# Kernel optimization log

Measured on AMD Instinct MI355X. Metric: run time of the kernel, lower is better.

Reference implementation:

```python
import jax, jax.numpy as jnp
import numpy as np

N = 50000      # nodes
E = 800000     # edges (before self loops)
D_IN = 256
D_H = 256
D_OUT = 64     # num_classes
SLOPE = 0.01   # leaky_relu slope


def setup_inputs() -> dict:
    key = jax.random.key(0)
    ks = jax.random.split(key, 8)
    x = jax.random.normal(ks[0], (N, D_IN), dtype=jnp.float32)
    edge_index = jax.random.randint(ks[1], (2, E), 0, N, dtype=jnp.int32)
    s = 0.05
    W1 = jax.random.normal(ks[2], (D_H, D_IN), dtype=jnp.float32) * s
    b1 = jnp.zeros((D_H,), dtype=jnp.float32)
    W2 = jax.random.normal(ks[3], (D_H, D_H), dtype=jnp.float32) * s
    b2 = jnp.zeros((D_H,), dtype=jnp.float32)
    W3 = jax.random.normal(ks[4], (D_OUT, D_H), dtype=jnp.float32) * s
    b3 = jnp.zeros((D_OUT,), dtype=jnp.float32)
    return {"x": x, "edge_index": edge_index, "W1": W1, "b1": b1,
            "W2": W2, "b2": b2, "W3": W3, "b3": b3}


def _gcn_layer(x, W, b, src, dst):
    # PyG GCNConv: h = x @ W^T; out[dst] += d^{-1/2}[src] d^{-1/2}[dst] * h[src]; out += b
    h = x @ W.T                                             # [N, out]
    ones = jnp.ones(src.shape[0], dtype=h.dtype)
    deg = jax.ops.segment_sum(ones, dst, num_segments=N)    # includes self loops
    dinv = jnp.where(deg > 0, jax.lax.rsqrt(deg), 0.0)
    norm = dinv[src] * dinv[dst]                            # [E+N]
    msg = h[src] * norm[:, None]                            # gather + scale
    out = jax.ops.segment_sum(msg, dst, num_segments=N)     # scatter-add
    return out + b


def reference(x, edge_index, W1, b1, W2, b2, W3, b3):
    src, dst = edge_index[0], edge_index[1]
    loop = jnp.arange(N, dtype=src.dtype)                   # add self loops
    src = jnp.concatenate([src, loop])
    dst = jnp.concatenate([dst, loop])
    act = lambda h: jax.nn.leaky_relu(h, negative_slope=SLOPE)
    h1 = act(_gcn_layer(x, W1, b1, src, dst))
    h2 = act(_gcn_layer(h1, W2, b2, src, dst))
    logits = _gcn_layer(h2, W3, b3, src, dst)               # no activation on last layer
    return (h1, h2, logits)
```

## Files before the change

kernel.cpp:

```cpp
#include <hip/hip_runtime.h>

#define N_NODES 50000
#define E_EDGES 800000
#define SLOPE 0.01f
#define CSTRIDE 32

typedef __attribute__((ext_vector_type(8))) short bf16x8;
typedef __attribute__((ext_vector_type(4))) float floatx4;
typedef __attribute__((ext_vector_type(4))) float f32x4;
typedef __attribute__((ext_vector_type(2))) float f32x2;
typedef __attribute__((ext_vector_type(2))) unsigned int u32x2;

__device__ __forceinline__ unsigned short f2bf(float f) {
    unsigned u = __builtin_bit_cast(unsigned, f);
    unsigned r = (u + 0x7FFFu + ((u >> 16) & 1u)) >> 16;
    return (unsigned short)r;
}
__device__ __forceinline__ float bf2f(unsigned short h) {
    unsigned u = ((unsigned)h) << 16;
    return __builtin_bit_cast(float, u);
}
__device__ __forceinline__ float blo(unsigned u) { return __builtin_bit_cast(float, u << 16); }
__device__ __forceinline__ float bhi(unsigned u) { return __builtin_bit_cast(float, u & 0xFFFF0000u); }
__device__ __forceinline__ f32x2 up2(unsigned u) {
    f32x2 t; t.x = blo(u); t.y = bhi(u); return t;
}

__device__ __forceinline__ void acc8p(uint4 v, f32x2 a[4]) {
    a[0] += up2(v.x); a[1] += up2(v.y); a[2] += up2(v.z); a[3] += up2(v.w);
}
__device__ __forceinline__ void acc4p(uint2 v, f32x2 a[2]) {
    a[0] += up2(v.x); a[1] += up2(v.y);
}


__device__ __forceinline__ void conv_body(const float* __restrict__ in,
                                          unsigned short* __restrict__ out, int i, int n4) {
    if (i < n4) {
        float4 v = ((const float4*)in)[i];
        ushort4 o;
        o.x = f2bf(v.x); o.y = f2bf(v.y); o.z = f2bf(v.z); o.w = f2bf(v.w);
        ((ushort4*)out)[i] = o;
    }
}

__device__ __forceinline__ void wfrag_body(const float* __restrict__ Wf,
                                           unsigned short* __restrict__ out, int idx, int n4) {
    if (idx >= n4) return;
    int n = idx >> 6;
    int k = (idx & 63) << 2;
    float4 v = ((const float4*)Wf)[idx];
    int jt = n >> 4, lm = n & 15, kk = k >> 5, q = (k >> 3) & 3, e = k & 7;
    int off = ((jt * 8 + kk) * 64 + q * 16 + lm) * 8 + e;
    ushort4 o;
    o.x = f2bf(v.x); o.y = f2bf(v.y); o.z = f2bf(v.z); o.w = f2bf(v.w);
    *(ushort4*)(out + off) = o;
}

#define PREP_HIST_B   3125
#define PREP_CONV_B   12500
#define PREP_W1_B     64
#define PREP_W2_B     64
#define PREP_W3_B     16
#define PREP_TOTAL_B  (PREP_HIST_B + PREP_CONV_B + PREP_W1_B + PREP_W2_B + PREP_W3_B)

__global__ __launch_bounds__(256) void prep0_kernel(
        const float* __restrict__ x, unsigned short* __restrict__ xb,
        const float* __restrict__ W1, unsigned short* __restrict__ W1f,
        const float* __restrict__ W2, unsigned short* __restrict__ W2f,
        const float* __restrict__ W3, unsigned short* __restrict__ W3f,
        const int* __restrict__ dst, int* __restrict__ counts,
        unsigned short* __restrict__ rank) {
    int b = blockIdx.x, tid = threadIdx.x;
    if (b < PREP_HIST_B) {
        int e = b * 256 + tid;
        if (e < E_EDGES) {
            int d = dst[e];
            rank[e] = (unsigned short)atomicAdd(&counts[(size_t)d * CSTRIDE], 1);
        }
    } else if (b < PREP_HIST_B + PREP_CONV_B) {
        conv_body(x, xb, (b - PREP_HIST_B) * 256 + tid, N_NODES * 256 / 4);
    } else if (b < PREP_HIST_B + PREP_CONV_B + PREP_W1_B) {
        wfrag_body(W1, W1f, (b - PREP_HIST_B - PREP_CONV_B) * 256 + tid, 16384);
    } else if (b < PREP_HIST_B + PREP_CONV_B + PREP_W1_B + PREP_W2_B) {
        wfrag_body(W2, W2f, (b - PREP_HIST_B - PREP_CONV_B - PREP_W1_B) * 256 + tid, 16384);
    } else {
        wfrag_body(W3, W3f, (b - PREP_HIST_B - PREP_CONV_B - PREP_W1_B - PREP_W2_B) * 256 + tid, 4096);
    }
}


#define SB 1024
__global__ __launch_bounds__(SB) void scan1_dinv_kernel(const int* __restrict__ counts,
                                                        int* __restrict__ partial,
                                                        int* __restrict__ bsum,
                                                        float* __restrict__ dinv) {
    __shared__ int wsum[16];
    int tid = threadIdx.x, lane = tid & 63, wid = tid >> 6;
    int i = blockIdx.x * SB + tid;
    int v = (i < N_NODES) ? counts[(size_t)i * CSTRIDE] : 0;
    int x = v;
    #pragma unroll
    for (int off = 1; off < 64; off <<= 1) {
        int y = __shfl_up(x, off, 64);
        if (lane >= off) x += y;
    }
    if (lane == 63) wsum[wid] = x;
    __syncthreads();
    if (wid == 0) {
        int s = (lane < 16) ? wsum[lane] : 0;
        #pragma unroll
        for (int off = 1; off < 16; off <<= 1) {
            int y = __shfl_up(s, off, 64);
            if (lane >= off) s += y;
        }
        if (lane < 16) wsum[lane] = s;
    }
    __syncthreads();
    int woff = wid ? wsum[wid - 1] : 0;
    if (i < N_NODES) {
        partial[i] = woff + x - v;
        dinv[i] = rsqrtf((float)(v + 1));
    }
    if (tid == SB - 1) bsum[blockIdx.x] = woff + x;
}

__global__ __launch_bounds__(256) void scan3b_kernel(int* __restrict__ row_ptr,
                                                     const int* __restrict__ bsum,
                                                     int nb) {
    __shared__ int pref[64];
    int tid = threadIdx.x;
    if (tid < 64) {
        int v = (tid < nb) ? bsum[tid] : 0;
        #pragma unroll
        for (int off = 1; off < 64; off <<= 1) {
            int y = __shfl_up(v, off, 64);
            if (tid >= off) v += y;
        }
        pref[tid] = v;
    }
    __syncthreads();
    int i = blockIdx.x * 256 + tid;
    if (i < N_NODES) {
        int c = i >> 10;
        int off = c ? pref[c - 1] : 0;
        row_ptr[i] += off;
    }
    if (i == 0) row_ptr[N_NODES] = pref[nb - 1];
}


template<int WAVES_M, int WAVES_N, int MT, int NT>
__device__ __forceinline__ void gemm_frag_body(
        int bx, int by, int tid,
        const unsigned short* __restrict__ Ab,
        const unsigned short* __restrict__ Bf,
        const float* __restrict__ dinv,
        unsigned short* __restrict__ C, int M, int Nc) {
    const int wave = tid >> 6, lane = tid & 63;
    const int lm = lane & 15, q = lane >> 4;
    const int bm = bx * (WAVES_M * MT * 16);
    const int bn = by * (WAVES_N * NT * 16);
    const int wm = (wave / WAVES_N) * (MT * 16);
    const int wn = (wave % WAVES_N) * (NT * 16);
    const int jt0 = (bn + wn) >> 4;

    const unsigned short* arow[MT];
    #pragma unroll
    for (int i = 0; i < MT; ++i) {
        int r = bm + wm + i * 16 + lm;
        if (r >= M) r = M - 1;
        arow[i] = Ab + (size_t)r * 256 + q * 8;
    }

    floatx4 acc[MT][NT] = {};

    #pragma unroll
    for (int kk = 0; kk < 8; ++kk) {
        bf16x8 a[MT], b[NT];
        #pragma unroll
        for (int i = 0; i < MT; ++i)
            a[i] = *(const bf16x8*)(arow[i] + kk * 32);
        #pragma unroll
        for (int j = 0; j < NT; ++j)
            b[j] = *(const bf16x8*)(Bf + (((jt0 + j) * 8 + kk) * 64 + lane) * 8);
        #pragma unroll
        for (int i = 0; i < MT; ++i)
            #pragma unroll
            for (int j = 0; j < NT; ++j)
                acc[i][j] = __builtin_amdgcn_mfma_f32_16x16x32_bf16(a[i], b[j], acc[i][j], 0, 0, 0);
    }

    #pragma unroll
    for (int i = 0; i < MT; ++i) {
        int rb = bm + wm + i * 16 + q * 4;
        #pragma unroll
        for (int r = 0; r < 4; ++r) {
            int row = rb + r;
            if (row < M) {
                float dd = dinv[row];
                #pragma unroll
                for (int j = 0; j < NT; ++j)
                    C[(size_t)row * Nc + bn + wn + j * 16 + lm] = f2bf(acc[i][j][r] * dd);
            }
        }
    }
}

__global__ __launch_bounds__(256) void gemm256_kernel(
        const unsigned short* __restrict__ Ab, const unsigned short* __restrict__ Bf,
        const float* __restrict__ dinv, unsigned short* __restrict__ C, int M, int Nc) {
    gemm_frag_body<2, 2, 4, 4>(blockIdx.x, blockIdx.y, threadIdx.x, Ab, Bf, dinv, C, M, Nc);
}

__global__ __launch_bounds__(256) void gemm64_kernel(
        const unsigned short* __restrict__ Ab, const unsigned short* __restrict__ Bf,
        const float* __restrict__ dinv, unsigned short* __restrict__ C, int M, int Nc) {
    gemm_frag_body<4, 1, 4, 4>(blockIdx.x, 0, threadIdx.x, Ab, Bf, dinv, C, M, Nc);
}

#define GEMM1_B 782
__global__ __launch_bounds__(256) void gemm1_place_kernel(
        const unsigned short* __restrict__ Ab, const unsigned short* __restrict__ Bf,
        const float* __restrict__ dinv, unsigned short* __restrict__ C, int M, int Nc,
        const int* __restrict__ src, const int* __restrict__ dst,
        const int* __restrict__ row_ptr, const unsigned short* __restrict__ rank,
        int* __restrict__ col_idx) {
    int b = blockIdx.x;
    if (b < PREP_HIST_B) {
        int e = b * 256 + threadIdx.x;
        if (e < E_EDGES) {
            int d = dst[e];
            int pos = row_ptr[d] + (int)rank[e];
            col_idx[pos] = src[e];
        }
    } else {
        int b2 = b - PREP_HIST_B;
        gemm_frag_body<2, 2, 4, 4>(b2 >> 1, b2 & 1, threadIdx.x, Ab, Bf, dinv, C, M, Nc);
    }
}


template<bool ACT>
__global__ __launch_bounds__(256) void agg256_kernel(
        const int* __restrict__ row_ptr, const int* __restrict__ col_idx,
        const float* __restrict__ dinv, const unsigned short* __restrict__ hs,
        const float* __restrict__ bias,
        float* __restrict__ out, unsigned short* __restrict__ outb) {
    int node = __builtin_amdgcn_readfirstlane(blockIdx.x * 4 + (threadIdx.x >> 6));
    int lane = threadIdx.x & 63;
    int half = lane >> 5, sl = lane & 31;

    f32x2 a[4] = {};

    int beg = row_ptr[node], end = row_ptr[node + 1];
    int j = beg;
    for (; j + 8 <= end; j += 8) {
        int s0 = col_idx[j + half];
        int s1 = col_idx[j + 2 + half];
        int s2 = col_idx[j + 4 + half];
        int s3 = col_idx[j + 6 + half];
        uint4 v0 = ((const uint4*)(hs + (size_t)s0 * 256))[sl];
        uint4 v1 = ((const uint4*)(hs + (size_t)s1 * 256))[sl];
        uint4 v2 = ((const uint4*)(hs + (size_t)s2 * 256))[sl];
        uint4 v3 = ((const uint4*)(hs + (size_t)s3 * 256))[sl];
        acc8p(v0, a); acc8p(v1, a); acc8p(v2, a); acc8p(v3, a);
    }
    for (; j + 2 <= end; j += 2) {
        int s = col_idx[j + half];
        uint4 v = ((const uint4*)(hs + (size_t)s * 256))[sl];
        acc8p(v, a);
    }
    if (j < end && half == 0) {
        int s = col_idx[j];
        uint4 v = ((const uint4*)(hs + (size_t)s * 256))[sl];
        acc8p(v, a);
    }

    float s0 = a[0].x, s1 = a[0].y, s2 = a[1].x, s3 = a[1].y;
    float s4 = a[2].x, s5 = a[2].y, s6 = a[3].x, s7 = a[3].y;

    s0 += __shfl_xor(s0, 32); s1 += __shfl_xor(s1, 32);
    s2 += __shfl_xor(s2, 32); s3 += __shfl_xor(s3, 32);
    s4 += __shfl_xor(s4, 32); s5 += __shfl_xor(s5, 32);
    s6 += __shfl_xor(s6, 32); s7 += __shfl_xor(s7, 32);

    uint4 sv = ((const uint4*)(hs + (size_t)node * 256))[sl];
    s0 += blo(sv.x); s1 += bhi(sv.x);
    s2 += blo(sv.y); s3 += bhi(sv.y);
    s4 += blo(sv.z); s5 += bhi(sv.z);
    s6 += blo(sv.w); s7 += bhi(sv.w);

    int srcl = lane >> 1;
    float t0 = __shfl(s0, srcl), t1 = __shfl(s1, srcl);
    float t2 = __shfl(s2, srcl), t3 = __shfl(s3, srcl);
    float t4 = __shfl(s4, srcl), t5 = __shfl(s5, srcl);
    float t6 = __shfl(s6, srcl), t7 = __shfl(s7, srcl);
    bool hi = (lane & 1);
    float f0 = hi ? t4 : t0, f1 = hi ? t5 : t1, f2 = hi ? t6 : t2, f3 = hi ? t7 : t3;

    float dd = dinv[node];
    const float4 b4 = ((const float4*)bias)[lane];
    f0 = fmaf(f0, dd, b4.x); f1 = fmaf(f1, dd, b4.y);
    f2 = fmaf(f2, dd, b4.z); f3 = fmaf(f3, dd, b4.w);
    if (ACT) {
        f0 = f0 > 0.f ? f0 : SLOPE * f0;
        f1 = f1 > 0.f ? f1 : SLOPE * f1;
        f2 = f2 > 0.f ? f2 : SLOPE * f2;
        f3 = f3 > 0.f ? f3 : SLOPE * f3;
    }
    f32x4 o = {f0, f1, f2, f3};
    __builtin_nontemporal_store(o, (f32x4*)(out + (size_t)node * 256) + lane);
    u32x2 obv;
    obv.x = ((unsigned)f2bf(f1) << 16) | f2bf(f0);
    obv.y = ((unsigned)f2bf(f3) << 16) | f2bf(f2);
    ((u32x2*)(outb + (size_t)node * 256))[lane] = obv;
}

__global__ __launch_bounds__(256) void agg64_kernel(
        const int* __restrict__ row_ptr, const int* __restrict__ col_idx,
        const float* __restrict__ dinv, const unsigned short* __restrict__ hs,
        const float* __restrict__ bias, float* __restrict__ out) {
    int node = __builtin_amdgcn_readfirstlane(blockIdx.x * 4 + (threadIdx.x >> 6));
    int lane = threadIdx.x & 63;
    int g = lane >> 4, sl = lane & 15;

    f32x2 a[2] = {};

    int beg = row_ptr[node], end = row_ptr[node + 1];
    int j = beg;
    for (; j + 8 <= end; j += 8) {
        int s0 = col_idx[j + g];
        int s1 = col_idx[j + 4 + g];
        uint2 v0 = ((const uint2*)(hs + (size_t)s0 * 64))[sl];
        uint2 v1 = ((const uint2*)(hs + (size_t)s1 * 64))[sl];
        acc4p(v0, a); acc4p(v1, a);
    }
    for (; j + 4 <= end; j += 4) {
        int s = col_idx[j + g];
        uint2 v = ((const uint2*)(hs + (size_t)s * 64))[sl];
        acc4p(v, a);
    }
    int rem = end - j;
    if (g < rem) {
        int s = col_idx[j + g];
        uint2 v = ((const uint2*)(hs + (size_t)s * 64))[sl];
        acc4p(v, a);
    }

    float s0 = a[0].x, s1 = a[0].y, s2 = a[1].x, s3 = a[1].y;

    s0 += __shfl_xor(s0, 16); s0 += __shfl_xor(s0, 32);
    s1 += __shfl_xor(s1, 16); s1 += __shfl_xor(s1, 32);
    s2 += __shfl_xor(s2, 16); s2 += __shfl_xor(s2, 32);
    s3 += __shfl_xor(s3, 16); s3 += __shfl_xor(s3, 32);

    uint2 sv = ((const uint2*)(hs + (size_t)node * 64))[sl];
    s0 += blo(sv.x); s1 += bhi(sv.x);
    s2 += blo(sv.y); s3 += bhi(sv.y);

    float dd = dinv[node];
    const float4 b4 = ((const float4*)bias)[sl];
    f32x4 o;
    o[0] = fmaf(s0, dd, b4.x);
    o[1] = fmaf(s1, dd, b4.y);
    o[2] = fmaf(s2, dd, b4.z);
    o[3] = fmaf(s3, dd, b4.w);
    if (g == 0)
        __builtin_nontemporal_store(o, (f32x4*)(out + (size_t)node * 64) + sl);
}


static inline int cdiv(long long a, long long b) { return (int)((a + b - 1) / b); }

extern "C" void kernel_launch(void* const* d_in, const int* in_sizes, int n_in,
                              void* d_out, int out_size, void* d_ws, size_t ws_size,
                              hipStream_t stream) {
    const float* x  = (const float*)d_in[0];
    const int* ei   = (const int*)d_in[1];
    const float* W1 = (const float*)d_in[2];
    const float* b1 = (const float*)d_in[3];
    const float* W2 = (const float*)d_in[4];
    const float* b2 = (const float*)d_in[5];
    const float* W3 = (const float*)d_in[6];
    const float* b3 = (const float*)d_in[7];

    const int* src = ei;
    const int* dst = ei + E_EDGES;

    char* ws = (char*)d_ws;
    int*   row_ptr = (int*)ws;   ws += 50112 * 4;
    float* dinv    = (float*)ws; ws += 50048 * 4;
    int*   bsum    = (int*)ws;   ws += 64 * 4;
    unsigned short* rank = (unsigned short*)ws; ws += (size_t)E_EDGES * 2;
    int*   col_idx = (int*)ws;   ws += (size_t)E_EDGES * 4;
    unsigned short* W1f = (unsigned short*)ws; ws += 65536 * 2;
    unsigned short* W2f = (unsigned short*)ws; ws += 65536 * 2;
    unsigned short* W3f = (unsigned short*)ws; ws += 16384 * 2;
    unsigned short* hb  = (unsigned short*)ws; ws += (size_t)N_NODES * 256 * 2;
    unsigned short* ob  = (unsigned short*)ws;

    int* counts = (int*)hb;

    float* out1 = (float*)d_out;
    float* out2 = out1 + (size_t)N_NODES * 256;
    float* out3 = out2 + (size_t)N_NODES * 256;

    const int NB = cdiv(N_NODES, SB);

    (void)hipMemsetAsync(counts, 0, (size_t)50048 * CSTRIDE * sizeof(int), stream);
    prep0_kernel<<<PREP_TOTAL_B, 256, 0, stream>>>(x, ob, W1, W1f, W2, W2f, W3, W3f,
                                                   dst, counts, rank);

    scan1_dinv_kernel<<<NB, SB, 0, stream>>>(counts, row_ptr, bsum, dinv);
    scan3b_kernel<<<cdiv(N_NODES, 256), 256, 0, stream>>>(row_ptr, bsum, NB);

    dim3 g256(cdiv(N_NODES, 128), 2);
    int agg_grid = cdiv(N_NODES, 4);

    gemm1_place_kernel<<<PREP_HIST_B + GEMM1_B, 256, 0, stream>>>(
        ob, W1f, dinv, hb, N_NODES, 256, src, dst, row_ptr, rank, col_idx);
    agg256_kernel<true><<<agg_grid, 256, 0, stream>>>(row_ptr, col_idx, dinv, hb, b1, out1, ob);

    gemm256_kernel<<<g256, 256, 0, stream>>>(ob, W2f, dinv, hb, N_NODES, 256);
    agg256_kernel<true><<<agg_grid, 256, 0, stream>>>(row_ptr, col_idx, dinv, hb, b2, out2, ob);

    gemm64_kernel<<<cdiv(N_NODES, 256), 256, 0, stream>>>(ob, W3f, dinv, hb, N_NODES, 64);
    agg64_kernel<<<agg_grid, 256, 0, stream>>>(row_ptr, col_idx, dinv, hb, b3, out3);
}
```

Measured before the change: 425.4 us.

## Fuse fp32-to-bf16 conversion into layer-1 GEMM and overlap it with degree histogram

The first GEMM now reads fp32 x directly and converts it to bf16 in registers, which removes the separate conversion pass and the bf16 copy of x. Because the GEMM no longer needs dinv, it runs in the same launch as the degree histogram, and the per-source degree scaling for layer 1 moves into the aggregation as a per-edge dinv gather. Edge placement becomes its own kernel, and the padded per-node atomic counters are packed densely. The trade-offs are extra dinv loads per edge in the first aggregation, more atomic contention on adjacent counters, and GEMM blocks reading fp32 rows directly from global memory.

Measured after the change: 426.2 us. About the same (+0.2%).

```diff
diff --git a/kernel.cpp b/kernel.cpp
--- a/kernel.cpp
+++ b/kernel.cpp
@@ -3,7 +3,6 @@
 #define N_NODES 50000
 #define E_EDGES 800000
 #define SLOPE 0.01f
-#define CSTRIDE 32
 
 typedef __attribute__((ext_vector_type(8))) short bf16x8;
 typedef __attribute__((ext_vector_type(4))) float floatx4;
@@ -32,16 +31,10 @@
 __device__ __forceinline__ void acc4p(uint2 v, f32x2 a[2]) {
     a[0] += up2(v.x); a[1] += up2(v.y);
 }
-
-
-__device__ __forceinline__ void conv_body(const float* __restrict__ in,
-                                          unsigned short* __restrict__ out, int i, int n4) {
-    if (i < n4) {
-        float4 v = ((const float4*)in)[i];
-        ushort4 o;
-        o.x = f2bf(v.x); o.y = f2bf(v.y); o.z = f2bf(v.z); o.w = f2bf(v.w);
-        ((ushort4*)out)[i] = o;
-    }
+__device__ __forceinline__ void acc8f(uint4 v, float d, f32x2 a[4]) {
+    f32x2 dv; dv.x = d; dv.y = d;
+    a[0] += up2(v.x) * dv; a[1] += up2(v.y) * dv;
+    a[2] += up2(v.z) * dv; a[3] += up2(v.w) * dv;
 }
 
 __device__ __forceinline__ void wfrag_body(const float* __restrict__ Wf,
@@ -57,35 +50,96 @@
     *(ushort4*)(out + off) = o;
 }
 
-#define PREP_HIST_B   3125
-#define PREP_CONV_B   12500
-#define PREP_W1_B     64
-#define PREP_W2_B     64
-#define PREP_W3_B     16
-#define PREP_TOTAL_B  (PREP_HIST_B + PREP_CONV_B + PREP_W1_B + PREP_W2_B + PREP_W3_B)
-
-__global__ __launch_bounds__(256) void prep0_kernel(
-        const float* __restrict__ x, unsigned short* __restrict__ xb,
+__global__ __launch_bounds__(256) void prep_w_kernel(
         const float* __restrict__ W1, unsigned short* __restrict__ W1f,
         const float* __restrict__ W2, unsigned short* __restrict__ W2f,
-        const float* __restrict__ W3, unsigned short* __restrict__ W3f,
+        const float* __restrict__ W3, unsigned short* __restrict__ W3f) {
+    int b = blockIdx.x, tid = threadIdx.x;
+    if (b < 64)       wfrag_body(W1, W1f, b * 256 + tid, 16384);
+    else if (b < 128) wfrag_body(W2, W2f, (b - 64) * 256 + tid, 16384);
+    else              wfrag_body(W3, W3f, (b - 128) * 256 + tid, 4096);
+}
+
+
+__device__ __forceinline__ void gemm1x_body(
+        int bx, int by, int tid,
+        const float* __restrict__ X,
+        const unsigned short* __restrict__ Bf,
+        unsigned short* __restrict__ C, int M, int Nc) {
+    const int wave = tid >> 6, lane = tid & 63;
+    const int lm = lane & 15, q = lane >> 4;
+    const int bm = bx * 128;
+    const int bn = by * 128;
+    const int wm = (wave >> 1) * 64;
+    const int wn = (wave & 1) * 64;
+    const int jt0 = (bn + wn) >> 4;
+
+    const float* xr[4];
+    #pragma unroll
+    for (int i = 0; i < 4; ++i) {
+        int r = bm + wm + i * 16 + lm;
+        if (r >= M) r = M - 1;
+        xr[i] = X + (size_t)r * 256 + q * 8;
+    }
+
+    floatx4 acc[4][4] = {};
+
+    #pragma unroll
+    for (int kk = 0; kk < 8; ++kk) {
+        bf16x8 a[4], b[4];
+        #pragma unroll
+        for (int i = 0; i < 4; ++i) {
+            float4 v0 = *(const float4*)(xr[i] + kk * 32);
+            float4 v1 = *(const float4*)(xr[i] + kk * 32 + 4);
+            bf16x8 t;
+            t[0] = (short)f2bf(v0.x); t[1] = (short)f2bf(v0.y);
+            t[2] = (short)f2bf(v0.z); t[3] = (short)f2bf(v0.w);
+            t[4] = (short)f2bf(v1.x); t[5] = (short)f2bf(v1.y);
+            t[6] = (short)f2bf(v1.z); t[7] = (short)f2bf(v1.w);
+            a[i] = t;
+        }
+        #pragma unroll
+        for (int j = 0; j < 4; ++j)
+            b[j] = *(const bf16x8*)(Bf + (((jt0 + j) * 8 + kk) * 64 + lane) * 8);
+        #pragma unroll
+        for (int i = 0; i < 4; ++i)
+            #pragma unroll
+            for (int j = 0; j < 4; ++j)
+                acc[i][j] = __builtin_amdgcn_mfma_f32_16x16x32_bf16(a[i], b[j], acc[i][j], 0, 0, 0);
+    }
+
+    #pragma unroll
+    for (int i = 0; i < 4; ++i) {
+        int rb = bm + wm + i * 16 + q * 4;
+        #pragma unroll
+        for (int r = 0; r < 4; ++r) {
+            int row = rb + r;
+            if (row < M) {
+                #pragma unroll
+                for (int j = 0; j < 4; ++j)
+                    C[(size_t)row * Nc + bn + wn + j * 16 + lm] = f2bf(acc[i][j][r]);
+            }
+        }
+    }
+}
+
+#define HIST_B 3125
+#define G1X_B  782
+__global__ __launch_bounds__(256) void gemm1x_hist_kernel(
+        const float* __restrict__ x, const unsigned short* __restrict__ W1f,
+        unsigned short* __restrict__ hb,
         const int* __restrict__ dst, int* __restrict__ counts,
         unsigned short* __restrict__ rank) {
-    int b = blockIdx.x, tid = threadIdx.x;
-    if (b < PREP_HIST_B) {
-        int e = b * 256 + tid;
+    int b = blockIdx.x;
+    if (b < HIST_B) {
+        int e = b * 256 + threadIdx.x;
         if (e < E_EDGES) {
             int d = dst[e];
-            rank[e] = (unsigned short)atomicAdd(&counts[(size_t)d * CSTRIDE], 1);
-        }
-    } else if (b < PREP_HIST_B + PREP_CONV_B) {
-        conv_body(x, xb, (b - PREP_HIST_B) * 256 + tid, N_NODES * 256 / 4);
-    } else if (b < PREP_HIST_B + PREP_CONV_B + PREP_W1_B) {
-        wfrag_body(W1, W1f, (b - PREP_HIST_B - PREP_CONV_B) * 256 + tid, 16384);
-    } else if (b < PREP_HIST_B + PREP_CONV_B + PREP_W1_B + PREP_W2_B) {
-        wfrag_body(W2, W2f, (b - PREP_HIST_B - PREP_CONV_B - PREP_W1_B) * 256 + tid, 16384);
+            rank[e] = (unsigned short)atomicAdd(&counts[d], 1);
+        }
     } else {
-        wfrag_body(W3, W3f, (b - PREP_HIST_B - PREP_CONV_B - PREP_W1_B - PREP_W2_B) * 256 + tid, 4096);
+        int b2 = b - HIST_B;
+        gemm1x_body(b2 >> 1, b2 & 1, threadIdx.x, x, W1f, hb, N_NODES, 256);
     }
 }
 
@@ -98,7 +152,7 @@
     __shared__ int wsum[16];
     int tid = threadIdx.x, lane = tid & 63, wid = tid >> 6;
     int i = blockIdx.x * SB + tid;
-    int v = (i < N_NODES) ? counts[(size_t)i * CSTRIDE] : 0;
+    int v = (i < N_NODES) ? counts[i] : 0;
     int x = v;
     #pragma unroll
     for (int off = 1; off < 64; off <<= 1) {
@@ -147,6 +201,17 @@
         row_ptr[i] += off;
     }
     if (i == 0) row_ptr[N_NODES] = pref[nb - 1];
+}
+
+__global__ __launch_bounds__(256) void place_kernel(
+        const int* __restrict__ src, const int* __restrict__ dst,
+        const int* __restrict__ row_ptr, const unsigned short* __restrict__ rank,
+        int* __restrict__ col_idx) {
+    int e = blockIdx.x * 256 + threadIdx.x;
+    if (e < E_EDGES) {
+        int d = dst[e];
+        col_idx[row_ptr[d] + (int)rank[e]] = src[e];
+    }
 }
 
 
@@ -219,29 +284,8 @@
     gemm_frag_body<4, 1, 4, 4>(blockIdx.x, 0, threadIdx.x, Ab, Bf, dinv, C, M, Nc);
 }
 
-#define GEMM1_B 782
-__global__ __launch_bounds__(256) void gemm1_place_kernel(
-        const unsigned short* __restrict__ Ab, const unsigned short* __restrict__ Bf,
-        const float* __restrict__ dinv, unsigned short* __restrict__ C, int M, int Nc,
-        const int* __restrict__ src, const int* __restrict__ dst,
-        const int* __restrict__ row_ptr, const unsigned short* __restrict__ rank,
-        int* __restrict__ col_idx) {
-    int b = blockIdx.x;
-    if (b < PREP_HIST_B) {
-        int e = b * 256 + threadIdx.x;
-        if (e < E_EDGES) {
-            int d = dst[e];
-            int pos = row_ptr[d] + (int)rank[e];
-            col_idx[pos] = src[e];
-        }
-    } else {
-        int b2 = b - PREP_HIST_B;
-        gemm_frag_body<2, 2, 4, 4>(b2 >> 1, b2 & 1, threadIdx.x, Ab, Bf, dinv, C, M, Nc);
-    }
-}
-
-
-template<bool ACT>
+
+template<bool ACT, bool ESCALE>
 __global__ __launch_bounds__(256) void agg256_kernel(
         const int* __restrict__ row_ptr, const int* __restrict__ col_idx,
         const float* __restrict__ dinv, const unsigned short* __restrict__ hs,
@@ -251,6 +295,7 @@
     int lane = threadIdx.x & 63;
     int half = lane >> 5, sl = lane & 31;
 
+    float dd = dinv[node];
     f32x2 a[4] = {};
 
     int beg = row_ptr[node], end = row_ptr[node + 1];
@@ -264,17 +309,22 @@
         uint4 v1 = ((const uint4*)(hs + (size_t)s1 * 256))[sl];
         uint4 v2 = ((const uint4*)(hs + (size_t)s2 * 256))[sl];
         uint4 v3 = ((const uint4*)(hs + (size_t)s3 * 256))[sl];
-        acc8p(v0, a); acc8p(v1, a); acc8p(v2, a); acc8p(v3, a);
+        if (ESCALE) {
+            acc8f(v0, dinv[s0], a); acc8f(v1, dinv[s1], a);
+            acc8f(v2, dinv[s2], a); acc8f(v3, dinv[s3], a);
+        } else {
+            acc8p(v0, a); acc8p(v1, a); acc8p(v2, a); acc8p(v3, a);
+        }
     }
     for (; j + 2 <= end; j += 2) {
         int s = col_idx[j + half];
         uint4 v = ((const uint4*)(hs + (size_t)s * 256))[sl];
-        acc8p(v, a);
+        if (ESCALE) acc8f(v, dinv[s], a); else acc8p(v, a);
     }
     if (j < end && half == 0) {
         int s = col_idx[j];
         uint4 v = ((const uint4*)(hs + (size_t)s * 256))[sl];
-        acc8p(v, a);
+        if (ESCALE) acc8f(v, dinv[s], a); else acc8p(v, a);
     }
 
     float s0 = a[0].x, s1 = a[0].y, s2 = a[1].x, s3 = a[1].y;
@@ -286,10 +336,11 @@
     s6 += __shfl_xor(s6, 32); s7 += __shfl_xor(s7, 32);
 
     uint4 sv = ((const uint4*)(hs + (size_t)node * 256))[sl];
-    s0 += blo(sv.x); s1 += bhi(sv.x);
-    s2 += blo(sv.y); s3 += bhi(sv.y);
-    s4 += blo(sv.z); s5 += bhi(sv.z);
-    s6 += blo(sv.w); s7 += bhi(sv.w);
+    float sf = ESCALE ? dd : 1.0f;
+    s0 = fmaf(blo(sv.x), sf, s0); s1 = fmaf(bhi(sv.x), sf, s1);
+    s2 = fmaf(blo(sv.y), sf, s2); s3 = fmaf(bhi(sv.y), sf, s3);
+    s4 = fmaf(blo(sv.z), sf, s4); s5 = fmaf(bhi(sv.z), sf, s5);
+    s6 = fmaf(blo(sv.w), sf, s6); s7 = fmaf(bhi(sv.w), sf, s7);
 
     int srcl = lane >> 1;
     float t0 = __shfl(s0, srcl), t1 = __shfl(s1, srcl);
@@ -299,7 +350,6 @@
     bool hi = (lane & 1);
     float f0 = hi ? t4 : t0, f1 = hi ? t5 : t1, f2 = hi ? t6 : t2, f3 = hi ? t7 : t3;
 
-    float dd = dinv[node];
     const float4 b4 = ((const float4*)bias)[lane];
     f0 = fmaf(f0, dd, b4.x); f1 = fmaf(f1, dd, b4.y);
     f2 = fmaf(f2, dd, b4.z); f3 = fmaf(f3, dd, b4.w);
@@ -400,7 +450,7 @@
     unsigned short* hb  = (unsigned short*)ws; ws += (size_t)N_NODES * 256 * 2;
     unsigned short* ob  = (unsigned short*)ws;
 
-    int* counts = (int*)hb;
+    int* counts = (int*)ob;
 
     float* out1 = (float*)d_out;
     float* out2 = out1 + (size_t)N_NODES * 256;
@@ -408,22 +458,22 @@
 
     const int NB = cdiv(N_NODES, SB);
 
-    (void)hipMemsetAsync(counts, 0, (size_t)50048 * CSTRIDE * sizeof(int), stream);
-    prep0_kernel<<<PREP_TOTAL_B, 256, 0, stream>>>(x, ob, W1, W1f, W2, W2f, W3, W3f,
-                                                   dst, counts, rank);
+    (void)hipMemsetAsync(counts, 0, 50048 * sizeof(int), stream);
+    prep_w_kernel<<<144, 256, 0, stream>>>(W1, W1f, W2, W2f, W3, W3f);
+
+    gemm1x_hist_kernel<<<HIST_B + G1X_B, 256, 0, stream>>>(x, W1f, hb, dst, counts, rank);
 
     scan1_dinv_kernel<<<NB, SB, 0, stream>>>(counts, row_ptr, bsum, dinv);
     scan3b_kernel<<<cdiv(N_NODES, 256), 256, 0, stream>>>(row_ptr, bsum, NB);
+    place_kernel<<<HIST_B, 256, 0, stream>>>(src, dst, row_ptr, rank, col_idx);
 
     dim3 g256(cdiv(N_NODES, 128), 2);
     int agg_grid = cdiv(N_NODES, 4);
 
-    gemm1_place_kernel<<<PREP_HIST_B + GEMM1_B, 256, 0, stream>>>(
-        ob, W1f, dinv, hb, N_NODES, 256, src, dst, row_ptr, rank, col_idx);
-    agg256_kernel<true><<<agg_grid, 256, 0, stream>>>(row_ptr, col_idx, dinv, hb, b1, out1, ob);
+    agg256_kernel<true, true><<<agg_grid, 256, 0, stream>>>(row_ptr, col_idx, dinv, hb, b1, out1, ob);
 
     gemm256_kernel<<<g256, 256, 0, stream>>>(ob, W2f, dinv, hb, N_NODES, 256);
-    agg256_kernel<true><<<agg_grid, 256, 0, stream>>>(row_ptr, col_idx, dinv, hb, b2, out2, ob);
+    agg256_kernel<true, false><<<agg_grid, 256, 0, stream>>>(row_ptr, col_idx, dinv, hb, b2, out2, ob);
 
     gemm64_kernel<<<cdiv(N_NODES, 256), 256, 0, stream>>>(ob, W3f, dinv, hb, N_NODES, 64);
     agg64_kernel<<<agg_grid, 256, 0, stream>>>(row_ptr, col_idx, dinv, hb, b3, out3);
```

## Pack degree counters densely and stage neighbor indices via wave shuffles

Applied to the files above, without the earlier changes.

Removes the 32-int stride padding on per-node degree counters, so the memset shrinks from about 6.4MB to 200KB and the scan reads contiguous counts. Atomics on neighboring nodes now share cache lines, which may add contention. In both aggregation kernels, each wave loads up to 64 column indices with one coalesced load and hands them to lanes with __shfl, replacing the repeated scalar index loads in the gather loops. The shuffle path adds ALU work and a chunked outer loop.

After: 421.4 us. Within noise of the previous version (-0.9%).

```diff
diff --git a/kernel.cpp b/kernel.cpp
--- a/kernel.cpp
+++ b/kernel.cpp
@@ -3,7 +3,6 @@
 #define N_NODES 50000
 #define E_EDGES 800000
 #define SLOPE 0.01f
-#define CSTRIDE 32
 
 typedef __attribute__((ext_vector_type(8))) short bf16x8;
 typedef __attribute__((ext_vector_type(4))) float floatx4;
@@ -76,7 +75,7 @@
         int e = b * 256 + tid;
         if (e < E_EDGES) {
             int d = dst[e];
-            rank[e] = (unsigned short)atomicAdd(&counts[(size_t)d * CSTRIDE], 1);
+            rank[e] = (unsigned short)atomicAdd(&counts[d], 1);
         }
     } else if (b < PREP_HIST_B + PREP_CONV_B) {
         conv_body(x, xb, (b - PREP_HIST_B) * 256 + tid, N_NODES * 256 / 4);
@@ -98,7 +97,7 @@
     __shared__ int wsum[16];
     int tid = threadIdx.x, lane = tid & 63, wid = tid >> 6;
     int i = blockIdx.x * SB + tid;
-    int v = (i < N_NODES) ? counts[(size_t)i * CSTRIDE] : 0;
+    int v = (i < N_NODES) ? counts[i] : 0;
     int x = v;
     #pragma unroll
     for (int off = 1; off < 64; off <<= 1) {
@@ -231,8 +230,7 @@
         int e = b * 256 + threadIdx.x;
         if (e < E_EDGES) {
             int d = dst[e];
-            int pos = row_ptr[d] + (int)rank[e];
-            col_idx[pos] = src[e];
+            col_idx[row_ptr[d] + (int)rank[e]] = src[e];
         }
     } else {
         int b2 = b - PREP_HIST_B;
@@ -254,27 +252,34 @@
     f32x2 a[4] = {};
 
     int beg = row_ptr[node], end = row_ptr[node + 1];
-    int j = beg;
-    for (; j + 8 <= end; j += 8) {
-        int s0 = col_idx[j + half];
-        int s1 = col_idx[j + 2 + half];
-        int s2 = col_idx[j + 4 + half];
-        int s3 = col_idx[j + 6 + half];
-        uint4 v0 = ((const uint4*)(hs + (size_t)s0 * 256))[sl];
-        uint4 v1 = ((const uint4*)(hs + (size_t)s1 * 256))[sl];
-        uint4 v2 = ((const uint4*)(hs + (size_t)s2 * 256))[sl];
-        uint4 v3 = ((const uint4*)(hs + (size_t)s3 * 256))[sl];
-        acc8p(v0, a); acc8p(v1, a); acc8p(v2, a); acc8p(v3, a);
-    }
-    for (; j + 2 <= end; j += 2) {
-        int s = col_idx[j + half];
-        uint4 v = ((const uint4*)(hs + (size_t)s * 256))[sl];
-        acc8p(v, a);
-    }
-    if (j < end && half == 0) {
-        int s = col_idx[j];
-        uint4 v = ((const uint4*)(hs + (size_t)s * 256))[sl];
-        acc8p(v, a);
+    for (int cbeg = beg; cbeg < end; cbeg += 64) {
+        int clen = end - cbeg; if (clen > 64) clen = 64;
+        int cidx = (lane < clen) ? col_idx[cbeg + lane] : 0;
+
+        int jj = 0;
+        for (; jj + 8 <= clen; jj += 8) {
+            int s0 = __shfl(cidx, jj + half);
+            int s1 = __shfl(cidx, jj + 2 + half);
+            int s2 = __shfl(cidx, jj + 4 + half);
+            int s3 = __shfl(cidx, jj + 6 + half);
+            uint4 v0 = ((const uint4*)(hs + (size_t)s0 * 256))[sl];
+            uint4 v1 = ((const uint4*)(hs + (size_t)s1 * 256))[sl];
+            uint4 v2 = ((const uint4*)(hs + (size_t)s2 * 256))[sl];
+            uint4 v3 = ((const uint4*)(hs + (size_t)s3 * 256))[sl];
+            acc8p(v0, a); acc8p(v1, a); acc8p(v2, a); acc8p(v3, a);
+        }
+        for (; jj + 2 <= clen; jj += 2) {
+            int s = __shfl(cidx, jj + half);
+            uint4 v = ((const uint4*)(hs + (size_t)s * 256))[sl];
+            acc8p(v, a);
+        }
+        if (jj < clen) {
+            int s = __shfl(cidx, jj);
+            if (half == 0) {
+                uint4 v = ((const uint4*)(hs + (size_t)s * 256))[sl];
+                acc8p(v, a);
+            }
+        }
     }
 
     float s0 = a[0].x, s1 = a[0].y, s2 = a[1].x, s3 = a[1].y;
@@ -328,24 +333,31 @@
     f32x2 a[2] = {};
 
     int beg = row_ptr[node], end = row_ptr[node + 1];
-    int j = beg;
-    for (; j + 8 <= end; j += 8) {
-        int s0 = col_idx[j + g];
-        int s1 = col_idx[j + 4 + g];
-        uint2 v0 = ((const uint2*)(hs + (size_t)s0 * 64))[sl];
-        uint2 v1 = ((const uint2*)(hs + (size_t)s1 * 64))[sl];
-        acc4p(v0, a); acc4p(v1, a);
-    }
-    for (; j + 4 <= end; j += 4) {
-        int s = col_idx[j + g];
-        uint2 v = ((const uint2*)(hs + (size_t)s * 64))[sl];
-        acc4p(v, a);
-    }
-    int rem = end - j;
-    if (g < rem) {
-        int s = col_idx[j + g];
-        uint2 v = ((const uint2*)(hs + (size_t)s * 64))[sl];
-        acc4p(v, a);
+    for (int cbeg = beg; cbeg < end; cbeg += 64) {
+        int clen = end - cbeg; if (clen > 64) clen = 64;
+        int cidx = (lane < clen) ? col_idx[cbeg + lane] : 0;
+
+        int jj = 0;
+        for (; jj + 8 <= clen; jj += 8) {
+            int s0 = __shfl(cidx, jj + g);
+            int s1 = __shfl(cidx, jj + 4 + g);
+            uint2 v0 = ((const uint2*)(hs + (size_t)s0 * 64))[sl];
+            uint2 v1 = ((const uint2*)(hs + (size_t)s1 * 64))[sl];
+            acc4p(v0, a); acc4p(v1, a);
+        }
+        for (; jj + 4 <= clen; jj += 4) {
+            int s = __shfl(cidx, jj + g);
+            uint2 v = ((const uint2*)(hs + (size_t)s * 64))[sl];
+            acc4p(v, a);
+        }
+        int rem = clen - jj;
+        if (rem > 0) {
+            int s = __shfl(cidx, jj + g);
+            if (g < rem) {
+                uint2 v = ((const uint2*)(hs + (size_t)s * 64))[sl];
+                acc4p(v, a);
+            }
+        }
     }
 
     float s0 = a[0].x, s1 = a[0].y, s2 = a[1].x, s3 = a[1].y;
@@ -408,7 +420,7 @@
 
     const int NB = cdiv(N_NODES, SB);
 
-    (void)hipMemsetAsync(counts, 0, (size_t)50048 * CSTRIDE * sizeof(int), stream);
+    (void)hipMemsetAsync(counts, 0, 50048 * sizeof(int), stream);
     prep0_kernel<<<PREP_TOTAL_B, 256, 0, stream>>>(x, ob, W1, W1f, W2, W2f, W3, W3f,
                                                    dst, counts, rank);
 
```
